# Performance work log

Measured on AMD Instinct MI355X. Metric: run time of the kernel, lower is better.

The kernel has to match this reference:

```python
import jax, jax.numpy as jnp
import numpy as np


def setup_inputs() -> dict:
    key = jax.random.key(0)
    k1, k2 = jax.random.split(key)
    source = jax.random.normal(k1, (8, 64, 128, 128), dtype=jnp.float32)
    flow_field = jax.random.normal(k2, (8, 2, 128, 128), dtype=jnp.float32)
    return {"source": source, "flow_field": flow_field, "kernel_size": 3}


def _block_extract(source, flow_field, K):
    # Semantics of block_extractor_cuda (GFLA/FFWM kernel):
    # output[b,c,y,x] = bilinear sample of source at
    #   y_s = (y//K) + flow[b,0,y//K,x//K] + (y%K - rad)
    #   x_s = (x//K) + flow[b,1,y//K,x//K] + (x%K - rad)
    # with corner indices clamped to the image border.
    B, C, Hs, Ws = source.shape
    _, _, Hf, Wf = flow_field.shape
    rad = (K - 1) // 2

    y = jnp.arange(K * Hf)
    x = jnp.arange(K * Wf)
    yf_idx = y // K                                  # flow row per output row
    xf_idx = x // K                                  # flow col per output col
    y_off = (y % K - rad).astype(jnp.float32)        # in-block offset
    x_off = (x % K - rad).astype(jnp.float32)

    flow_y = flow_field[:, 0]                        # (B,Hf,Wf)
    flow_x = flow_field[:, 1]
    fy = flow_y[:, yf_idx][:, :, xf_idx]             # (B,K*Hf,K*Wf)
    fx = flow_x[:, yf_idx][:, :, xf_idx]

    ys = yf_idx.astype(jnp.float32)[None, :, None] + y_off[None, :, None] + fy
    xs = xf_idx.astype(jnp.float32)[None, None, :] + x_off[None, None, :] + fx

    yT = jnp.clip(jnp.floor(ys).astype(jnp.int32), 0, Hs - 1)
    yB = jnp.clip(yT + 1, 0, Hs - 1)
    xL = jnp.clip(jnp.floor(xs).astype(jnp.int32), 0, Ws - 1)
    xR = jnp.clip(xL + 1, 0, Ws - 1)

    dy = ys - yT.astype(jnp.float32)                 # weights vs clamped floor (as in CUDA)
    dx = xs - xL.astype(jnp.float32)

    def gather(yi, xi):
        # source (B,C,Hs,Ws), yi/xi (B,Ho,Wo) -> (B,C,Ho,Wo)
        return jax.vmap(lambda s, yy, xx: s[:, yy, xx])(source, yi, xi)

    tl = gather(yT, xL)
    tr = gather(yT, xR)
    bl = gather(yB, xL)
    br = gather(yB, xR)

    wtl = ((1.0 - dy) * (1.0 - dx))[:, None]
    wtr = ((1.0 - dy) * dx)[:, None]
    wbl = (dy * (1.0 - dx))[:, None]
    wbr = (dy * dx)[:, None]
    return tl * wtl + tr * wtr + bl * wbl + br * wbr


def reference(source, flow_field, kernel_size):
    return _block_extract(source, flow_field, int(kernel_size))
```

## Files before the change

kernel.cpp:

```cpp
#include <hip/hip_runtime.h>

constexpr int Bc = 8, Cc = 64, Hs = 128, Ws = 128, Kk = 3;
constexpr int HO = Kk * Hs;
constexpr int WO = Kk * Ws;
constexpr int WG = 768;
constexpr int SP = 132;
constexpr int BAND = Hs / 2;

__global__ __launch_bounds__(WG, 6) void block_extract_lds(
    const float* __restrict__ src, const float* __restrict__ flow,
    float* __restrict__ out)
{
    __shared__ float plane[(Hs + 1) * SP];

    const int wg  = blockIdx.x;
    const int b   = wg >> 6;
    const int tid = threadIdx.x;

    const float* splane = src + (size_t)wg * (Hs * Ws);
    const float4* sp4 = (const float4*)splane;
    for (int i = tid; i < (Hs + 1) * (Ws / 4); i += WG) {
        const int r = i >> 5, j = i & 31;
        const int sr = (r < Hs) ? r : (Hs - 1);
        *(float4*)(plane + r * SP + 4 * j) = sp4[sr * (Ws / 4) + j];
    }
    for (int r = tid; r <= Hs; r += WG) {
        const int sr = (r < Hs) ? r : (Hs - 1);
        plane[r * SP + Ws] = splane[sr * Ws + (Ws - 1)];
    }
    __syncthreads();

    const int band = (tid >= 384) ? 1 : 0;
    const int X    = tid - band * 384;
    const int y0   = band * BAND;
    const int y1   = y0 + BAND;

    const int xf = X / 3;
    const float xconst = (float)(X - 2 * xf - 1);

    const float* flowy = flow + (size_t)b * 2 * Hs * Ws;
    const float* flowx = flowy + Hs * Ws;
    float* outcol = out + (size_t)wg * (HO * WO) + X;

    float fy = flowy[y0 * Ws + xf];
    float fx = flowx[y0 * Ws + xf];

    for (int yf = y0; yf < y1; ++yf) {
        const int nr = (yf < y1 - 1 ? yf + 1 : yf) * Ws + xf;
        const float fy_n = flowy[nr];
        const float fx_n = flowx[nr];

        const float ys0 = (float)(yf - 1) + fy;
        const int   F   = (int)floorf(ys0);

        const float xs = xconst + fx;
        int xL = (int)floorf(xs);
        xL = min(max(xL, 0), Ws - 1);
        const float dx  = xs - (float)xL;
        const float wx0 = 1.0f - dx;

        float* orow = outcol + (size_t)(3 * yf) * WO;
        #pragma unroll
        for (int k = 0; k < 3; ++k) {
            const int   yT  = min(max(F + k, 0), Hs - 1);
            const float dy  = ys0 + (float)k - (float)yT;
            const float wy0 = 1.0f - dy;
            const float* p = plane + yT * SP + xL;
            const float tl = p[0];
            const float tr = p[1];
            const float bl = p[SP];
            const float br = p[SP + 1];
            const float v = (tl * wx0 + tr * dx) * wy0
                          + (bl * wx0 + br * dx) * dy;
            __builtin_nontemporal_store(v, orow + (size_t)k * WO);
        }
        fy = fy_n;
        fx = fx_n;
    }
}

extern "C" void kernel_launch(void* const* d_in, const int* in_sizes, int n_in,
                              void* d_out, int out_size, void* d_ws, size_t ws_size,
                              hipStream_t stream) {
    const float* src  = (const float*)d_in[0];
    const float* flow = (const float*)d_in[1];
    float* out = (float*)d_out;

    dim3 block(WG);
    dim3 grid(Bc * Cc);
    block_extract_lds<<<grid, block, 0, stream>>>(src, flow, out);
}
```

Before: 362.9 us.

## Share LDS rows across the three vertical taps using extrapolated padded borders

```diff
diff --git a/kernel.cpp b/kernel.cpp
--- a/kernel.cpp
+++ b/kernel.cpp
@@ -4,29 +4,54 @@
 constexpr int HO = Kk * Hs;
 constexpr int WO = Kk * Ws;
 constexpr int WG = 768;
-constexpr int SP = 132;
+constexpr int SP = 136;
+constexpr int ROWS = 133;
 constexpr int BAND = Hs / 2;
 
 __global__ __launch_bounds__(WG, 6) void block_extract_lds(
     const float* __restrict__ src, const float* __restrict__ flow,
     float* __restrict__ out)
 {
-    __shared__ float plane[(Hs + 1) * SP];
+    __shared__ float plane[ROWS * SP];
 
     const int wg  = blockIdx.x;
     const int b   = wg >> 6;
     const int tid = threadIdx.x;
 
     const float* splane = src + (size_t)wg * (Hs * Ws);
+
     const float4* sp4 = (const float4*)splane;
-    for (int i = tid; i < (Hs + 1) * (Ws / 4); i += WG) {
+    for (int i = tid; i < Hs * (Ws / 4); i += WG) {
         const int r = i >> 5, j = i & 31;
-        const int sr = (r < Hs) ? r : (Hs - 1);
-        *(float4*)(plane + r * SP + 4 * j) = sp4[sr * (Ws / 4) + j];
+        *(float4*)(plane + (r + 2) * SP + 4 + 4 * j) = sp4[i];
     }
-    for (int r = tid; r <= Hs; r += WG) {
-        const int sr = (r < Hs) ? r : (Hs - 1);
-        plane[r * SP + Ws] = splane[sr * Ws + (Ws - 1)];
+    for (int r = tid; r < Hs; r += WG) {
+        const float a = splane[r * Ws];
+        const float b2 = splane[r * Ws + 1];
+        plane[(r + 2) * SP + 3]   = 2.0f * a - b2;
+        plane[(r + 2) * SP + 132] = splane[r * Ws + 127];
+    }
+    for (int t = tid; t < 5 * 130; t += WG) {
+        const int g  = t / 130;
+        const int cc = t % 130;
+        const int c  = cc - 1;
+        float v;
+        int rmem;
+        if (g < 2) {
+            const float e0 = (c == -1) ? 2.0f * splane[0] - splane[1]
+                           : (c == 128) ? splane[127] : splane[c];
+            const float e1 = (c == -1) ? 2.0f * splane[Ws] - splane[Ws + 1]
+                           : (c == 128) ? splane[Ws + 127] : splane[Ws + c];
+            v = (g == 0) ? 3.0f * e0 - 2.0f * e1
+                         : 2.0f * e0 - e1;
+            rmem = g;
+        } else {
+            const float* r127 = splane + 127 * Ws;
+            v = (c == -1) ? 2.0f * r127[0] - r127[1]
+              : (c == 128) ? r127[127] : r127[c];
+            rmem = 128 + g;
+        }
+        plane[rmem * SP + cc + 3] = v;
     }
     __syncthreads();
 
@@ -40,40 +65,46 @@
 
     const float* flowy = flow + (size_t)b * 2 * Hs * Ws;
     const float* flowx = flowy + Hs * Ws;
-    float* outcol = out + (size_t)wg * (HO * WO) + X;
+    float* orow = out + (size_t)wg * (HO * WO) + X + (size_t)(3 * y0) * WO;
 
     float fy = flowy[y0 * Ws + xf];
     float fx = flowx[y0 * Ws + xf];
 
+    #pragma unroll 2
     for (int yf = y0; yf < y1; ++yf) {
         const int nr = (yf < y1 - 1 ? yf + 1 : yf) * Ws + xf;
         const float fy_n = flowy[nr];
         const float fx_n = flowx[nr];
 
         const float ys0 = (float)(yf - 1) + fy;
-        const int   F   = (int)floorf(ys0);
+        float Ff = floorf(ys0);
+        Ff = fminf(fmaxf(Ff, -2.0f), 127.0f);
+        const float d  = ys0 - Ff;
+        const float w0 = 1.0f - d;
 
         const float xs = xconst + fx;
-        int xL = (int)floorf(xs);
-        xL = min(max(xL, 0), Ws - 1);
-        const float dx  = xs - (float)xL;
-        const float wx0 = 1.0f - dx;
+        float xLf = floorf(xs);
+        xLf = fminf(fmaxf(xLf, -1.0f), 127.0f);
+        const float dx = xs - xLf;
+        const float wx = 1.0f - dx;
 
-        float* orow = outcol + (size_t)(3 * yf) * WO;
-        #pragma unroll
-        for (int k = 0; k < 3; ++k) {
-            const int   yT  = min(max(F + k, 0), Hs - 1);
-            const float dy  = ys0 + (float)k - (float)yT;
-            const float wy0 = 1.0f - dy;
-            const float* p = plane + yT * SP + xL;
-            const float tl = p[0];
-            const float tr = p[1];
-            const float bl = p[SP];
-            const float br = p[SP + 1];
-            const float v = (tl * wx0 + tr * dx) * wy0
-                          + (bl * wx0 + br * dx) * dy;
-            __builtin_nontemporal_store(v, orow + (size_t)k * WO);
-        }
+        const float* p = plane + ((int)Ff + 2) * SP + ((int)xLf + 4);
+        const float r0a = p[0],  r0b = p[1];
+        const float r1a = p[SP], r1b = p[SP + 1];
+        const float* q = p + 2 * SP;
+        const float r2a = q[0],  r2b = q[1];
+        const float r3a = q[SP], r3b = q[SP + 1];
+
+        const float h0 = r0a * wx + r0b * dx;
+        const float h1 = r1a * wx + r1b * dx;
+        const float h2 = r2a * wx + r2b * dx;
+        const float h3 = r3a * wx + r3b * dx;
+
+        __builtin_nontemporal_store(h0 * w0 + h1 * d, orow);
+        __builtin_nontemporal_store(h1 * w0 + h2 * d, orow + WO);
+        __builtin_nontemporal_store(h2 * w0 + h3 * d, orow + 2 * WO);
+
+        orow += 3 * WO;
         fy = fy_n;
         fx = fx_n;
     }
```

Result: faster. 339.5 us (-6.4%).
